# Kernel tuning notes

Measured on AMD Instinct MI355X. Metric: run time of the kernel, lower is better.

The kernel has to match this reference:

```python
import jax, jax.numpy as jnp
import numpy as np

B, T, C, D = 8, 4096, 1024, 64  # batch, block_size, input_dim, output_dim


def setup_inputs() -> dict:
    key = jax.random.key(0)
    kx, kk, kq, kv = jax.random.split(key, 4)
    s = 1.0 / np.sqrt(C)  # nn.Linear default init range scale
    X = jax.random.normal(kx, (B, T, C), dtype=jnp.float32)
    Wk = jax.random.uniform(kk, (D, C), jnp.float32, -s, s) * 0.01  # key weight scaled by 0.01 per __post_init__
    Wq = jax.random.uniform(kq, (D, C), jnp.float32, -s, s)
    Wv = jax.random.uniform(kv, (D, C), jnp.float32, -s, s)
    return {"X": X, "Wk": Wk, "Wq": Wq, "Wv": Wv}


def reference(X, Wk, Wq, Wv):
    # bias-free linear projections (torch Linear: X @ W.T)
    keys = jnp.einsum('btc,dc->btd', X, Wk)
    queries = jnp.einsum('btc,dc->btd', X, Wq)
    values = jnp.einsum('btc,dc->btd', X, Wv)
    # scaled dot-product logits [B, T, T]
    logits = jnp.einsum('btd,bsd->bts', queries, keys) / jnp.sqrt(jnp.float32(D))
    causal = jnp.tril(jnp.ones((T, T), dtype=bool))
    logits = jnp.where(causal[None, :, :], logits, -jnp.inf)
    affinities = jax.nn.softmax(logits, axis=2)  # dropout_frac=0.0 -> identity
    return jnp.einsum('bts,bsd->btd', affinities, values)
```

## Files before the change

kernel.cpp:

```cpp
#include <hip/hip_runtime.h>


typedef short bf16x8 __attribute__((ext_vector_type(8)));
typedef short bf16x4 __attribute__((ext_vector_type(4)));
typedef float f32x4  __attribute__((ext_vector_type(4)));

static __device__ __forceinline__ short f2bf(float x) {
    union { float f; unsigned u; } v; v.f = x;
    return (short)((v.u + 0x7fffu + ((v.u >> 16) & 1u)) >> 16);
}

__global__ __launch_bounds__(64) void pack_w_kernel(
    const float* __restrict__ Wk, const float* __restrict__ Wq,
    const float* __restrict__ Wv, short* __restrict__ Wp)
{
    const int c    = blockIdx.x;
    const int lane = threadIdx.x;
    const int k2   = c & 1;
    const int m    = (c >> 1) % 3;
    const int ksw  = c / 6;
    const int ks   = ksw & 15;
    const int w    = ksw >> 4;
    const int l15  = lane & 15;
    const int quad = lane >> 4;
    const float* W = (m == 0) ? Wk : (m == 1) ? Wq : Wv;
    const float sc = (m == 1) ? 0.18033688f : 1.0f;
    const float* p = W + (long)(w * 16 + l15) * 1024 + ks * 64 + k2 * 32 + quad * 8;
    f32x4 a = *(const f32x4*)(p);
    f32x4 b = *(const f32x4*)(p + 4);
    bf16x8 f;
#pragma unroll
    for (int j = 0; j < 4; ++j) { f[j] = f2bf(a[j] * sc); f[j + 4] = f2bf(b[j] * sc); }
    *(bf16x8*)(Wp + (long)c * 512 + lane * 8) = f;
}

__global__ __launch_bounds__(256, 2) void proj_kernel(
    const float* __restrict__ X,
    const short* __restrict__ Wp,
    short* __restrict__ Kb,
    short* __restrict__ Qb,
    short* __restrict__ Vt)
{
    __shared__ __align__(16) short xs[2][64 * 72];
    const int tid  = threadIdx.x;
    const int w    = tid >> 6;
    const int lane = tid & 63;
    const int l15  = lane & 15;
    const int quad = lane >> 4;
    const int t0   = blockIdx.x * 64;

    const int rowA = tid >> 3, colg = tid & 7;
    const int rowB = rowA + 32;
    const float* xpA = X + (long)(t0 + rowA) * 1024 + colg * 8;
    const float* xpB = X + (long)(t0 + rowB) * 1024 + colg * 8;
    const int lwA = rowA * 72 + colg * 8;
    const int lwB = rowB * 72 + colg * 8;

    const short* wp = Wp + (long)(w * 16) * 6 * 512 + lane * 8;

    f32x4 acc[4][3];
#pragma unroll
    for (int rt = 0; rt < 4; ++rt)
#pragma unroll
        for (int m = 0; m < 3; ++m) { acc[rt][m][0]=0.f; acc[rt][m][1]=0.f; acc[rt][m][2]=0.f; acc[rt][m][3]=0.f; }

    f32x4 xr[2][4];
    bf16x8 wfc[3][2], wfn[3][2];

    {
#pragma unroll
        for (int s = 0; s < 2; ++s) {
            const int k0 = s * 64;
            xr[s][0] = *(const f32x4*)(xpA + k0);
            xr[s][1] = *(const f32x4*)(xpA + k0 + 4);
            xr[s][2] = *(const f32x4*)(xpB + k0);
            xr[s][3] = *(const f32x4*)(xpB + k0 + 4);
        }
#pragma unroll
        for (int m = 0; m < 3; ++m)
#pragma unroll
            for (int k2 = 0; k2 < 2; ++k2)
                wfc[m][k2] = *(const bf16x8*)(wp + (m * 2 + k2) * 512);
        bf16x8 c0, c1;
#pragma unroll
        for (int j = 0; j < 4; ++j) { c0[j] = f2bf(xr[0][0][j]); c0[j+4] = f2bf(xr[0][1][j]);
                                      c1[j] = f2bf(xr[0][2][j]); c1[j+4] = f2bf(xr[0][3][j]); }
        *(bf16x8*)(&xs[0][lwA]) = c0;
        *(bf16x8*)(&xs[0][lwB]) = c1;
    }
    __syncthreads();

#pragma unroll 2
    for (int ks = 0; ks < 16; ++ks) {
        const int buf = ks & 1;
        if (ks < 14) {
            const int k0 = (ks + 2) * 64;
            xr[buf][0] = *(const f32x4*)(xpA + k0);
            xr[buf][1] = *(const f32x4*)(xpA + k0 + 4);
            xr[buf][2] = *(const f32x4*)(xpB + k0);
            xr[buf][3] = *(const f32x4*)(xpB + k0 + 4);
        }
        if (ks < 15) {
            const int cb = (ks + 1) * 6;
#pragma unroll
            for (int m = 0; m < 3; ++m)
#pragma unroll
                for (int k2 = 0; k2 < 2; ++k2)
                    wfn[m][k2] = *(const bf16x8*)(wp + (cb + m * 2 + k2) * 512);
        }
#pragma unroll
        for (int k2 = 0; k2 < 2; ++k2)
#pragma unroll
            for (int rt = 0; rt < 4; ++rt) {
                bf16x8 a = *(const bf16x8*)(&xs[buf][(rt * 16 + l15) * 72 + k2 * 32 + quad * 8]);
#pragma unroll
                for (int m = 0; m < 3; ++m)
                    acc[rt][m] = __builtin_amdgcn_mfma_f32_16x16x32_bf16(a, wfc[m][k2], acc[rt][m], 0, 0, 0);
            }
        if (ks < 15) {
            const int nset = (ks + 1) & 1;
            bf16x8 c0, c1;
#pragma unroll
            for (int j = 0; j < 4; ++j) { c0[j] = f2bf(xr[nset][0][j]); c0[j+4] = f2bf(xr[nset][1][j]);
                                          c1[j] = f2bf(xr[nset][2][j]); c1[j+4] = f2bf(xr[nset][3][j]); }
            *(bf16x8*)(&xs[nset][lwA]) = c0;
            *(bf16x8*)(&xs[nset][lwB]) = c1;
        }
        __syncthreads();
#pragma unroll
        for (int m = 0; m < 3; ++m)
#pragma unroll
            for (int k2 = 0; k2 < 2; ++k2) wfc[m][k2] = wfn[m][k2];
    }

    const int d    = w * 16 + l15;
    const int bidx = t0 >> 12;
#pragma unroll
    for (int rt = 0; rt < 4; ++rt) {
        const int tf = t0 + rt * 16 + quad * 4;
#pragma unroll
        for (int r = 0; r < 4; ++r) Kb[(long)(tf + r) * 64 + d] = f2bf(acc[rt][0][r]);
#pragma unroll
        for (int r = 0; r < 4; ++r) Qb[(long)(tf + r) * 64 + d] = f2bf(acc[rt][1][r]);
        bf16x4 pv;
#pragma unroll
        for (int r = 0; r < 4; ++r) pv[r] = f2bf(acc[rt][2][r]);
        *(bf16x4*)(Vt + ((long)bidx * 64 + d) * 4096 + (tf & 4095)) = pv;
    }
}

__global__ __launch_bounds__(256, 2) void flash_kernel(
    const short* __restrict__ Qb,
    const short* __restrict__ Kb,
    const short* __restrict__ Vt,
    float* __restrict__ Out)
{
    __shared__ __align__(16) char smem[33280];
    short* ps = (short*)smem;
    float* os = (float*)smem;
    float* ls = (float*)(smem + 32768);

    const int tid  = threadIdx.x;
    const int w    = tid >> 6;
    const int lane = tid & 63;
    const int l15  = lane & 15;
    const int quad = lane >> 4;
    const int b    = blockIdx.x & 7;
    const int tile = 127 - (blockIdx.x >> 3);
    const int t0   = tile * 32;

    const int nkb = (t0 >> 6) + 1;
    const int len = (nkb + 3) >> 2;
    const int kb0 = w * len;
    const int kb1 = (kb0 + len < nkb) ? (kb0 + len) : nkb;

    const short* Kbase = Kb + (long)b * 4096 * 64;
    const short* Vbase = Vt + (long)b * 64 * 4096;

    bf16x8 aq[2][2];
#pragma unroll
    for (int q2 = 0; q2 < 2; ++q2) {
        const long qoff = ((long)b * 4096 + t0 + q2 * 16 + l15) * 64;
        aq[q2][0] = *(const bf16x8*)(Qb + qoff + quad * 8);
        aq[q2][1] = *(const bf16x8*)(Qb + qoff + 32 + quad * 8);
    }

    bf16x8 bones;
#pragma unroll
    for (int j = 0; j < 8; ++j) bones[j] = (l15 == 0) ? (short)0x3F80 : (short)0;

    f32x4 o[2][4], lacc[2];
#pragma unroll
    for (int q2 = 0; q2 < 2; ++q2) {
        lacc[q2][0]=0.f; lacc[q2][1]=0.f; lacc[q2][2]=0.f; lacc[q2][3]=0.f;
#pragma unroll
        for (int dt = 0; dt < 4; ++dt) { o[q2][dt][0]=0.f; o[q2][dt][1]=0.f; o[q2][dt][2]=0.f; o[q2][dt][3]=0.f; }
    }

    bf16x8 kc[4][2], kn[4][2];
    if (kb0 < kb1) {
        const int s0 = kb0 << 6;
#pragma unroll
        for (int ct = 0; ct < 4; ++ct) {
            const short* kp = Kbase + (long)(s0 + ct * 16 + l15) * 64 + quad * 8;
            kc[ct][0] = *(const bf16x8*)(kp);
            kc[ct][1] = *(const bf16x8*)(kp + 32);
        }
    }

    for (int kb = kb0; kb < kb1; ++kb) {
        const int s0 = kb << 6;

        bf16x8 vf[4][2];
#pragma unroll
        for (int dt = 0; dt < 4; ++dt) {
            const short* vp = Vbase + (long)(dt * 16 + l15) * 4096 + s0 + quad * 8;
            vf[dt][0] = *(const bf16x8*)(vp);
            vf[dt][1] = *(const bf16x8*)(vp + 32);
        }
        if (kb + 1 < kb1) {
            const int sn = s0 + 64;
#pragma unroll
            for (int ct = 0; ct < 4; ++ct) {
                const short* kp = Kbase + (long)(sn + ct * 16 + l15) * 64 + quad * 8;
                kn[ct][0] = *(const bf16x8*)(kp);
                kn[ct][1] = *(const bf16x8*)(kp + 32);
            }
        }

#pragma unroll
        for (int q2 = 0; q2 < 2; ++q2) {
            short* myps = ps + ((w << 1) | q2) * 1152;
            f32x4 st[4];
#pragma unroll
            for (int ct = 0; ct < 4; ++ct) {
                f32x4 z; z[0]=0.f; z[1]=0.f; z[2]=0.f; z[3]=0.f;
                z = __builtin_amdgcn_mfma_f32_16x16x32_bf16(aq[q2][0], kc[ct][0], z, 0, 0, 0);
                st[ct] = __builtin_amdgcn_mfma_f32_16x16x32_bf16(aq[q2][1], kc[ct][1], st[ct] = z, 0, 0, 0);
            }
            if (kb == nkb - 1) {
#pragma unroll
                for (int ct = 0; ct < 4; ++ct) {
                    const int s = s0 + ct * 16 + l15;
#pragma unroll
                    for (int r = 0; r < 4; ++r)
                        if (s > t0 + q2 * 16 + quad * 4 + r) st[ct][r] = -1e30f;
                }
            }
#pragma unroll
            for (int ct = 0; ct < 4; ++ct)
#pragma unroll
                for (int r = 0; r < 4; ++r)
                    myps[(quad * 4 + r) * 72 + ct * 16 + l15] =
                        f2bf(__builtin_amdgcn_exp2f(st[ct][r]));
            bf16x8 ap0 = *(const bf16x8*)(myps + l15 * 72 + quad * 8);
            bf16x8 ap1 = *(const bf16x8*)(myps + l15 * 72 + 32 + quad * 8);
            lacc[q2] = __builtin_amdgcn_mfma_f32_16x16x32_bf16(ap0, bones, lacc[q2], 0, 0, 0);
            lacc[q2] = __builtin_amdgcn_mfma_f32_16x16x32_bf16(ap1, bones, lacc[q2], 0, 0, 0);
#pragma unroll
            for (int dt = 0; dt < 4; ++dt) {
                o[q2][dt] = __builtin_amdgcn_mfma_f32_16x16x32_bf16(ap0, vf[dt][0], o[q2][dt], 0, 0, 0);
                o[q2][dt] = __builtin_amdgcn_mfma_f32_16x16x32_bf16(ap1, vf[dt][1], o[q2][dt], 0, 0, 0);
            }
        }
#pragma unroll
        for (int ct = 0; ct < 4; ++ct) { kc[ct][0] = kn[ct][0]; kc[ct][1] = kn[ct][1]; }
    }

    __syncthreads();
#pragma unroll
    for (int q2 = 0; q2 < 2; ++q2) {
#pragma unroll
        for (int dt = 0; dt < 4; ++dt)
#pragma unroll
            for (int r = 0; r < 4; ++r)
                os[w * 2048 + (q2 * 16 + quad * 4 + r) * 64 + dt * 16 + l15] = o[q2][dt][r];
        if (l15 == 0) {
#pragma unroll
            for (int r = 0; r < 4; ++r) ls[w * 32 + q2 * 16 + quad * 4 + r] = lacc[q2][r];
        }
    }
    __syncthreads();

    const int row = tid >> 3, c0 = (tid & 7) * 8;
    f32x4 a0, a1; a0[0]=0.f;a0[1]=0.f;a0[2]=0.f;a0[3]=0.f; a1=a0;
    float lsum = 0.f;
#pragma unroll
    for (int w2 = 0; w2 < 4; ++w2) {
        f32x4 v0 = *(const f32x4*)(os + w2 * 2048 + row * 64 + c0);
        f32x4 v1 = *(const f32x4*)(os + w2 * 2048 + row * 64 + c0 + 4);
        a0[0]+=v0[0]; a0[1]+=v0[1]; a0[2]+=v0[2]; a0[3]+=v0[3];
        a1[0]+=v1[0]; a1[1]+=v1[1]; a1[2]+=v1[2]; a1[3]+=v1[3];
        lsum += ls[w2 * 32 + row];
    }
    const float inv = 1.0f / lsum;
    f32x4 r0, r1;
    r0[0]=a0[0]*inv; r0[1]=a0[1]*inv; r0[2]=a0[2]*inv; r0[3]=a0[3]*inv;
    r1[0]=a1[0]*inv; r1[1]=a1[1]*inv; r1[2]=a1[2]*inv; r1[3]=a1[3]*inv;
    float* op = Out + ((long)b * 4096 + t0 + row) * 64 + c0;
    *(f32x4*)(op)     = r0;
    *(f32x4*)(op + 4) = r1;
}

extern "C" void kernel_launch(void* const* d_in, const int* in_sizes, int n_in,
                              void* d_out, int out_size, void* d_ws, size_t ws_size,
                              hipStream_t stream) {
    const float* X  = (const float*)d_in[0];
    const float* Wk = (const float*)d_in[1];
    const float* Wq = (const float*)d_in[2];
    const float* Wv = (const float*)d_in[3];

    short* ws = (short*)d_ws;
    const long NE = (long)8 * 4096 * 64;
    short* Qb = ws;
    short* Kb = ws + NE;
    short* Vt = ws + 2 * NE;
    short* Wpk = ws + 3 * NE;

    pack_w_kernel<<<384, 64, 0, stream>>>(Wk, Wq, Wv, Wpk);
    proj_kernel<<<512, 256, 0, stream>>>(X, Wpk, Kb, Qb, Vt);
    flash_kernel<<<1024, 256, 0, stream>>>(Qb, Kb, Vt, (float*)d_out);
}
```

Measured before the change: 276.6 us.

## Split projection K-dimension across waves with LDS atomic reduction

The projection kernel now has each of the four waves handle a quarter of the 1024-wide reduction dimension for all 192 output columns of a 32-row tile, instead of splitting the output columns across waves. X is loaded straight into registers and converted to bf16 without the shared-memory staging and the per-step barriers. The partial sums are combined with float atomics in shared memory, then written out coalesced. The grid doubles to 1024 blocks. The cost is more accumulator registers, weight fragments read from global memory in every iteration, and LDS atomic contention.

```diff
diff --git a/kernel.cpp b/kernel.cpp
--- a/kernel.cpp
+++ b/kernel.cpp
@@ -20,12 +20,12 @@
     const int m    = (c >> 1) % 3;
     const int ksw  = c / 6;
     const int ks   = ksw & 15;
-    const int w    = ksw >> 4;
+    const int wq   = ksw >> 4;
     const int l15  = lane & 15;
     const int quad = lane >> 4;
     const float* W = (m == 0) ? Wk : (m == 1) ? Wq : Wv;
     const float sc = (m == 1) ? 0.18033688f : 1.0f;
-    const float* p = W + (long)(w * 16 + l15) * 1024 + ks * 64 + k2 * 32 + quad * 8;
+    const float* p = W + (long)(wq * 16 + l15) * 1024 + ks * 64 + k2 * 32 + quad * 8;
     f32x4 a = *(const f32x4*)(p);
     f32x4 b = *(const f32x4*)(p + 4);
     bf16x8 f;
@@ -34,6 +34,7 @@
     *(bf16x8*)(Wp + (long)c * 512 + lane * 8) = f;
 }
 
+#define RSTRIDE 204
 __global__ __launch_bounds__(256, 2) void proj_kernel(
     const float* __restrict__ X,
     const short* __restrict__ Wp,
@@ -41,111 +42,109 @@
     short* __restrict__ Qb,
     short* __restrict__ Vt)
 {
-    __shared__ __align__(16) short xs[2][64 * 72];
+    __shared__ __align__(16) float rs[32 * RSTRIDE];
     const int tid  = threadIdx.x;
     const int w    = tid >> 6;
     const int lane = tid & 63;
     const int l15  = lane & 15;
     const int quad = lane >> 4;
-    const int t0   = blockIdx.x * 64;
-
-    const int rowA = tid >> 3, colg = tid & 7;
-    const int rowB = rowA + 32;
-    const float* xpA = X + (long)(t0 + rowA) * 1024 + colg * 8;
-    const float* xpB = X + (long)(t0 + rowB) * 1024 + colg * 8;
-    const int lwA = rowA * 72 + colg * 8;
-    const int lwB = rowB * 72 + colg * 8;
-
-    const short* wp = Wp + (long)(w * 16) * 6 * 512 + lane * 8;
-
-    f32x4 acc[4][3];
-#pragma unroll
-    for (int rt = 0; rt < 4; ++rt)
-#pragma unroll
-        for (int m = 0; m < 3; ++m) { acc[rt][m][0]=0.f; acc[rt][m][1]=0.f; acc[rt][m][2]=0.f; acc[rt][m][3]=0.f; }
-
-    f32x4 xr[2][4];
-    bf16x8 wfc[3][2], wfn[3][2];
+    const int r0   = blockIdx.x * 32;
 
     {
-#pragma unroll
-        for (int s = 0; s < 2; ++s) {
-            const int k0 = s * 64;
-            xr[s][0] = *(const f32x4*)(xpA + k0);
-            xr[s][1] = *(const f32x4*)(xpA + k0 + 4);
-            xr[s][2] = *(const f32x4*)(xpB + k0);
-            xr[s][3] = *(const f32x4*)(xpB + k0 + 4);
-        }
-#pragma unroll
-        for (int m = 0; m < 3; ++m)
-#pragma unroll
-            for (int k2 = 0; k2 < 2; ++k2)
-                wfc[m][k2] = *(const bf16x8*)(wp + (m * 2 + k2) * 512);
-        bf16x8 c0, c1;
-#pragma unroll
-        for (int j = 0; j < 4; ++j) { c0[j] = f2bf(xr[0][0][j]); c0[j+4] = f2bf(xr[0][1][j]);
-                                      c1[j] = f2bf(xr[0][2][j]); c1[j+4] = f2bf(xr[0][3][j]); }
-        *(bf16x8*)(&xs[0][lwA]) = c0;
-        *(bf16x8*)(&xs[0][lwB]) = c1;
-    }
+        f32x4 z; z[0]=0.f; z[1]=0.f; z[2]=0.f; z[3]=0.f;
+#pragma unroll
+        for (int j = 0; j < 7; ++j) {
+            const int idx = tid + j * 256;
+            if (idx < (32 * RSTRIDE) / 4) ((f32x4*)rs)[idx] = z;
+        }
+    }
+
+    const float* xA = X + (long)(r0 + l15) * 1024 + quad * 8;
+    const float* xB = xA + 16 * 1024;
+    const short* wpb = Wp + lane * 8;
+
+    f32x4 acc[2][12];
+#pragma unroll
+    for (int rt = 0; rt < 2; ++rt)
+#pragma unroll
+        for (int c = 0; c < 12; ++c) { acc[rt][c][0]=0.f; acc[rt][c][1]=0.f; acc[rt][c][2]=0.f; acc[rt][c][3]=0.f; }
+
+    f32x4 xr[8];
+    {
+        const int kb = w * 256;
+        xr[0] = *(const f32x4*)(xA + kb);      xr[1] = *(const f32x4*)(xA + kb + 4);
+        xr[2] = *(const f32x4*)(xA + kb + 32); xr[3] = *(const f32x4*)(xA + kb + 36);
+        xr[4] = *(const f32x4*)(xB + kb);      xr[5] = *(const f32x4*)(xB + kb + 4);
+        xr[6] = *(const f32x4*)(xB + kb + 32); xr[7] = *(const f32x4*)(xB + kb + 36);
+    }
+
+#pragma unroll
+    for (int i = 0; i < 4; ++i) {
+        bf16x8 a[2][2];
+#pragma unroll
+        for (int rt = 0; rt < 2; ++rt)
+#pragma unroll
+            for (int k2 = 0; k2 < 2; ++k2) {
+                bf16x8 f;
+#pragma unroll
+                for (int j = 0; j < 4; ++j) {
+                    f[j]     = f2bf(xr[rt * 4 + k2 * 2][j]);
+                    f[j + 4] = f2bf(xr[rt * 4 + k2 * 2 + 1][j]);
+                }
+                a[rt][k2] = f;
+            }
+        if (i < 3) {
+            const int kb = (w * 4 + i + 1) * 64;
+            xr[0] = *(const f32x4*)(xA + kb);      xr[1] = *(const f32x4*)(xA + kb + 4);
+            xr[2] = *(const f32x4*)(xA + kb + 32); xr[3] = *(const f32x4*)(xA + kb + 36);
+            xr[4] = *(const f32x4*)(xB + kb);      xr[5] = *(const f32x4*)(xB + kb + 4);
+            xr[6] = *(const f32x4*)(xB + kb + 32); xr[7] = *(const f32x4*)(xB + kb + 36);
+        }
+        const int ks = w * 4 + i;
+#pragma unroll
+        for (int c = 0; c < 12; ++c) {
+            const short* bp = wpb + (size_t)(((c & 3) * 16 + ks) * 6 + (c >> 2) * 2) * 512;
+            bf16x8 b0 = *(const bf16x8*)(bp);
+            bf16x8 b1 = *(const bf16x8*)(bp + 512);
+            acc[0][c] = __builtin_amdgcn_mfma_f32_16x16x32_bf16(a[0][0], b0, acc[0][c], 0, 0, 0);
+            acc[0][c] = __builtin_amdgcn_mfma_f32_16x16x32_bf16(a[0][1], b1, acc[0][c], 0, 0, 0);
+            acc[1][c] = __builtin_amdgcn_mfma_f32_16x16x32_bf16(a[1][0], b0, acc[1][c], 0, 0, 0);
+            acc[1][c] = __builtin_amdgcn_mfma_f32_16x16x32_bf16(a[1][1], b1, acc[1][c], 0, 0, 0);
+        }
+    }
+
     __syncthreads();
-
-#pragma unroll 2
-    for (int ks = 0; ks < 16; ++ks) {
-        const int buf = ks & 1;
-        if (ks < 14) {
-            const int k0 = (ks + 2) * 64;
-            xr[buf][0] = *(const f32x4*)(xpA + k0);
-            xr[buf][1] = *(const f32x4*)(xpA + k0 + 4);
-            xr[buf][2] = *(const f32x4*)(xpB + k0);
-            xr[buf][3] = *(const f32x4*)(xpB + k0 + 4);
-        }
-        if (ks < 15) {
-            const int cb = (ks + 1) * 6;
-#pragma unroll
-            for (int m = 0; m < 3; ++m)
-#pragma unroll
-                for (int k2 = 0; k2 < 2; ++k2)
-                    wfn[m][k2] = *(const bf16x8*)(wp + (cb + m * 2 + k2) * 512);
-        }
-#pragma unroll
-        for (int k2 = 0; k2 < 2; ++k2)
-#pragma unroll
-            for (int rt = 0; rt < 4; ++rt) {
-                bf16x8 a = *(const bf16x8*)(&xs[buf][(rt * 16 + l15) * 72 + k2 * 32 + quad * 8]);
-#pragma unroll
-                for (int m = 0; m < 3; ++m)
-                    acc[rt][m] = __builtin_amdgcn_mfma_f32_16x16x32_bf16(a, wfc[m][k2], acc[rt][m], 0, 0, 0);
-            }
-        if (ks < 15) {
-            const int nset = (ks + 1) & 1;
-            bf16x8 c0, c1;
-#pragma unroll
-            for (int j = 0; j < 4; ++j) { c0[j] = f2bf(xr[nset][0][j]); c0[j+4] = f2bf(xr[nset][1][j]);
-                                          c1[j] = f2bf(xr[nset][2][j]); c1[j+4] = f2bf(xr[nset][3][j]); }
-            *(bf16x8*)(&xs[nset][lwA]) = c0;
-            *(bf16x8*)(&xs[nset][lwB]) = c1;
-        }
-        __syncthreads();
-#pragma unroll
-        for (int m = 0; m < 3; ++m)
-#pragma unroll
-            for (int k2 = 0; k2 < 2; ++k2) wfc[m][k2] = wfn[m][k2];
-    }
-
-    const int d    = w * 16 + l15;
-    const int bidx = t0 >> 12;
-#pragma unroll
-    for (int rt = 0; rt < 4; ++rt) {
-        const int tf = t0 + rt * 16 + quad * 4;
-#pragma unroll
-        for (int r = 0; r < 4; ++r) Kb[(long)(tf + r) * 64 + d] = f2bf(acc[rt][0][r]);
-#pragma unroll
-        for (int r = 0; r < 4; ++r) Qb[(long)(tf + r) * 64 + d] = f2bf(acc[rt][1][r]);
-        bf16x4 pv;
-#pragma unroll
-        for (int r = 0; r < 4; ++r) pv[r] = f2bf(acc[rt][2][r]);
-        *(bf16x4*)(Vt + ((long)bidx * 64 + d) * 4096 + (tf & 4095)) = pv;
+#pragma unroll
+    for (int rt = 0; rt < 2; ++rt)
+#pragma unroll
+        for (int c = 0; c < 12; ++c) {
+            float* dst = rs + (rt * 16 + quad * 4) * RSTRIDE + c * 16 + l15;
+#pragma unroll
+            for (int r = 0; r < 4; ++r)
+                atomicAdd(dst + r * RSTRIDE, acc[rt][c][r]);
+        }
+    __syncthreads();
+
+    {
+        const int row = tid >> 3, dq = tid & 7;
+        const float* src = rs + row * RSTRIDE + dq * 8;
+        f32x4 k0 = *(const f32x4*)(src);        f32x4 k1 = *(const f32x4*)(src + 4);
+        f32x4 q0 = *(const f32x4*)(src + 64);   f32x4 q1 = *(const f32x4*)(src + 68);
+        bf16x8 kk, qq;
+#pragma unroll
+        for (int j = 0; j < 4; ++j) { kk[j] = f2bf(k0[j]); kk[j + 4] = f2bf(k1[j]);
+                                      qq[j] = f2bf(q0[j]); qq[j + 4] = f2bf(q1[j]); }
+        *(bf16x8*)(Kb + (long)(r0 + row) * 64 + dq * 8) = kk;
+        *(bf16x8*)(Qb + (long)(r0 + row) * 64 + dq * 8) = qq;
+    }
+    {
+        const int d = tid >> 2, tg = tid & 3;
+        const int bidx = r0 >> 12;
+        bf16x8 vv;
+#pragma unroll
+        for (int j = 0; j < 8; ++j)
+            vv[j] = f2bf(rs[(tg * 8 + j) * RSTRIDE + 128 + d]);
+        *(bf16x8*)(Vt + ((long)bidx * 64 + d) * 4096 + (r0 & 4095) + tg * 8) = vv;
     }
 }
 
@@ -318,6 +317,6 @@
     short* Wpk = ws + 3 * NE;
 
     pack_w_kernel<<<384, 64, 0, stream>>>(Wk, Wq, Wv, Wpk);
-    proj_kernel<<<512, 256, 0, stream>>>(X, Wpk, Kb, Qb, Vt);
+    proj_kernel<<<1024, 256, 0, stream>>>(X, Wpk, Kb, Qb, Vt);
     flash_kernel<<<1024, 256, 0, stream>>>(Qb, Kb, Vt, (float*)d_out);
 }
```

Measured after the change: 410.9 us. +48.5%, slower.
